# Performance work log

Hardware: AMD Instinct MI355X
Metric: run time of the kernel (lower is better)

The kernel has to match this reference:

```python
import jax, jax.numpy as jnp
import numpy as np

B, P, H, W, K = 2, 4096, 128, 128, 8
RADIUS = 0.05  # NDC-space point radius (raster_settings.radius)


def setup_inputs() -> dict:
    key = jax.random.key(0)
    k1, k2, k3 = jax.random.split(key, 3)
    points_world = jax.random.normal(k1, (B, P, 3), jnp.float32)
    # near-identity rotation (row-vector convention: X_view = X_world @ R + T)
    R = jnp.eye(3, dtype=jnp.float32)[None] + 0.01 * jax.random.normal(k2, (B, 3, 3), jnp.float32)
    # translate cloud to z ~ +3 so points are in front of the camera
    T = (0.1 * jax.random.normal(k3, (B, 3), jnp.float32)).at[:, 2].add(3.0)
    focal = jnp.full((B,), 1.5, jnp.float32)
    return {"points_world": points_world, "R": R, "T": T, "focal": focal}


def reference(points_world, R, T, focal):
    # --- camera transform: world -> view -> NDC (z kept in view space) ---
    pts_view = jnp.einsum('bpi,bij->bpj', points_world, R) + T[:, None, :]  # [B,P,3]
    z = pts_view[..., 2]                                                    # [B,P]
    x_ndc = focal[:, None] * pts_view[..., 0] / z
    y_ndc = focal[:, None] * pts_view[..., 1] / z

    # --- pixel-center NDC grid (pytorch3d convention: +x left, +y up) ---
    gx = 1.0 - 2.0 * (jnp.arange(W, dtype=jnp.float32) + 0.5) / W  # [W]
    gy = 1.0 - 2.0 * (jnp.arange(H, dtype=jnp.float32) + 0.5) / H  # [H]
    GY, GX = jnp.meshgrid(gy, gx, indexing='ij')
    gxf = GX.reshape(-1)  # [HW]
    gyf = GY.reshape(-1)

    # --- per-pixel candidate search: squared NDC distance to every point ---
    dist2 = (gxf[None, :, None] - x_ndc[:, None, :]) ** 2 \
          + (gyf[None, :, None] - y_ndc[:, None, :]) ** 2      # [B,HW,P]
    inside = (dist2 < RADIUS * RADIUS) & (z[:, None, :] > 0.0)  # in radius & in front

    # --- depth-sorted top-K nearest-in-z among covering points ---
    keyz = jnp.where(inside, z[:, None, :], jnp.inf)            # [B,HW,P]
    neg_top, idx_top = jax.lax.top_k(-keyz, K)                  # K smallest z
    zk = jnp.take_along_axis(keyz, idx_top, axis=-1)            # [B,HW,K]
    dk = jnp.take_along_axis(dist2, idx_top, axis=-1)
    valid = jnp.isfinite(zk)

    idx = jnp.where(valid, idx_top, -1).reshape(B, H, W, K)
    zbuf = jnp.where(valid, zk, -1.0).reshape(B, H, W, K)
    dists = jnp.where(valid, dk, -1.0).reshape(B, H, W, K)
    return idx, zbuf, dists
```

## Files before the change

kernel.cpp:

```cpp
#include <hip/hip_runtime.h>
#include <math.h>

#define BB 2
#define PP 4096
#define HH 128
#define WW 128
#define KK 8
#define TS 8
#define NTX (WW / TS)
#define NTY (HH / TS)
#define NW 4
#define SEG (PP / NW)

__global__ __launch_bounds__(64 * NW, 2) void raster_kernel(
    const float* __restrict__ pw,
    const float* __restrict__ Rm,
    const float* __restrict__ Tv,
    const float* __restrict__ fo,
    float* __restrict__ out,
    int N)
{
    __shared__ float4 cand[NW][SEG];

    const int tx = blockIdx.x, ty = blockIdx.y, b = blockIdx.z;
    const int wv   = threadIdx.x >> 6;
    const int lane = threadIdx.x & 63;

    const float* r = Rm + b * 9;
    const float r00=r[0], r01=r[1], r02=r[2];
    const float r10=r[3], r11=r[4], r12=r[5];
    const float r20=r[6], r21=r[7], r22=r[8];
    const float t0=Tv[b*3+0], t1=Tv[b*3+1], t2=Tv[b*3+2];
    const float f = fo[b];

    const float R2f   = (float)(0.05 * 0.05);
    const float apron = 0.05f + 1e-5f;

    float gx_hi = 1.0f - 2.0f * ((float)(tx * TS)          + 0.5f) / (float)WW;
    float gx_lo = 1.0f - 2.0f * ((float)(tx * TS + TS - 1) + 0.5f) / (float)WW;
    float gy_hi = 1.0f - 2.0f * ((float)(ty * TS)          + 0.5f) / (float)HH;
    float gy_lo = 1.0f - 2.0f * ((float)(ty * TS + TS - 1) + 0.5f) / (float)HH;
    const float xmin = gx_lo - apron, xmax = gx_hi + apron;
    const float ymin = gy_lo - apron, ymax = gy_hi + apron;

    int cnt = 0;
    const float* pwb = pw + (size_t)b * PP * 3;
#pragma unroll 4
    for (int it = 0; it < SEG / 64; ++it) {
        int i = wv * SEG + it * 64 + lane;
        const float* q = pwb + i * 3;
        float x = q[0], y = q[1], z = q[2];
        float vx = __fadd_rn(__fadd_rn(__fadd_rn(__fmul_rn(x, r00), __fmul_rn(y, r10)), __fmul_rn(z, r20)), t0);
        float vy = __fadd_rn(__fadd_rn(__fadd_rn(__fmul_rn(x, r01), __fmul_rn(y, r11)), __fmul_rn(z, r21)), t1);
        float vz = __fadd_rn(__fadd_rn(__fadd_rn(__fmul_rn(x, r02), __fmul_rn(y, r12)), __fmul_rn(z, r22)), t2);
        float xn = __fmul_rn(f, vx) / vz;
        float yn = __fmul_rn(f, vy) / vz;
        bool keep = (vz > 0.0f) && (xn >= xmin) && (xn <= xmax)
                                && (yn >= ymin) && (yn <= ymax);
        unsigned long long m = __ballot(keep);
        if (keep) {
            int pos = __popcll(m & ((1ull << lane) - 1ull));
            cand[wv][cnt + pos] = make_float4(xn, yn, vz, __int_as_float(i));
        }
        cnt += __popcll(m);
    }

    int w = tx * TS + (lane & (TS - 1));
    int h = ty * TS + (lane / TS);
    float gx = 1.0f - 2.0f * ((float)w + 0.5f) / (float)WW;
    float gy = 1.0f - 2.0f * ((float)h + 0.5f) / (float)HH;

    float zk[KK], dk[KK]; int ik[KK];
#pragma unroll
    for (int j = 0; j < KK; ++j) { zk[j] = INFINITY; dk[j] = -1.0f; ik[j] = -1; }

    for (int s = 0; s < cnt; ++s) {
        float4 q = cand[wv][s];
        float dx = __fsub_rn(gx, q.x);
        float dy = __fsub_rn(gy, q.y);
        float d2 = __fadd_rn(__fmul_rn(dx, dx), __fmul_rn(dy, dy));
        float z = q.z;
        if (d2 < R2f && z < zk[KK - 1]) {
            int i = __float_as_int(q.w);
#pragma unroll
            for (int j = KK - 1; j >= 1; --j) {
                if (z < zk[j]) {
                    if (z < zk[j - 1]) { zk[j] = zk[j-1]; ik[j] = ik[j-1]; dk[j] = dk[j-1]; }
                    else               { zk[j] = z;       ik[j] = i;       dk[j] = d2;      }
                }
            }
            if (z < zk[0]) { zk[0] = z; ik[0] = i; dk[0] = d2; }
        }
    }

    __syncthreads();
    float* mz = (float*)&cand[0][0];
    float* mi = mz + NW * KK * 64;
    float* md = mi + NW * KK * 64;
#pragma unroll
    for (int s = 0; s < KK; ++s) {
        mz[(wv * KK + s) * 64 + lane] = zk[s];
        mi[(wv * KK + s) * 64 + lane] = __int_as_float(ik[s]);
        md[(wv * KK + s) * 64 + lane] = dk[s];
    }
    __syncthreads();

    if (wv == 0) {
        float hz[NW], hd[NW]; int hi_[NW], hp[NW];
#pragma unroll
        for (int wq = 0; wq < NW; ++wq) {
            hp[wq]  = 0;
            hz[wq]  = mz[(wq * KK) * 64 + lane];
            hi_[wq] = __float_as_int(mi[(wq * KK) * 64 + lane]);
            hd[wq]  = md[(wq * KK) * 64 + lane];
        }
        float A[KK], Z[KK], D[KK];
#pragma unroll
        for (int o = 0; o < KK; ++o) {
            int bw = 0;
#pragma unroll
            for (int wq = 1; wq < NW; ++wq) {
                bool better = (hz[wq] < hz[bw]) ||
                              ((hz[wq] == hz[bw]) && (hi_[wq] < hi_[bw]));
                if (better) bw = wq;
            }
            float sz = hz[0], sd = hd[0]; int si = hi_[0];
#pragma unroll
            for (int wq = 1; wq < NW; ++wq) {
                if (bw == wq) { sz = hz[wq]; sd = hd[wq]; si = hi_[wq]; }
            }
            A[o] = (float)si;
            Z[o] = (si >= 0) ? sz : -1.0f;
            D[o] = sd;
#pragma unroll
            for (int wq = 0; wq < NW; ++wq) {
                if (bw == wq) {
                    int p = ++hp[wq];
                    if (p < KK) {
                        hz[wq]  = mz[(wq * KK + p) * 64 + lane];
                        hi_[wq] = __float_as_int(mi[(wq * KK + p) * 64 + lane]);
                        hd[wq]  = md[(wq * KK + p) * 64 + lane];
                    } else {
                        hz[wq] = INFINITY; hi_[wq] = -1; hd[wq] = -1.0f;
                    }
                }
            }
        }
        int pix  = (b * HH + h) * WW + w;
        int base = pix * KK;
        float4* oa = (float4*)(out + base);
        float4* oz = (float4*)(out + N + base);
        float4* od = (float4*)(out + 2 * N + base);
        oa[0] = ((float4*)A)[0]; oa[1] = ((float4*)A)[1];
        oz[0] = ((float4*)Z)[0]; oz[1] = ((float4*)Z)[1];
        od[0] = ((float4*)D)[0]; od[1] = ((float4*)D)[1];
    }
}

extern "C" void kernel_launch(void* const* d_in, const int* in_sizes, int n_in,
                              void* d_out, int out_size, void* d_ws, size_t ws_size,
                              hipStream_t stream) {
    const float* pw = (const float*)d_in[0];
    const float* Rm = (const float*)d_in[1];
    const float* Tv = (const float*)d_in[2];
    const float* fo = (const float*)d_in[3];
    int N = out_size / 3;

    hipLaunchKernelGGL(raster_kernel, dim3(NTX, NTY, BB), dim3(64 * NW), 0, stream,
                       pw, Rm, Tv, fo, (float*)d_out, N);
}
```

Before: 88.97 us.

## Use eight waves per tile with capped candidate buffers and prefetched point loads

```diff
diff --git a/kernel.cpp b/kernel.cpp
--- a/kernel.cpp
+++ b/kernel.cpp
@@ -9,10 +9,12 @@
 #define TS 8
 #define NTX (WW / TS)
 #define NTY (HH / TS)
-#define NW 4
+#define NW 8
 #define SEG (PP / NW)
+#define CIT (SEG / 64)
+#define CAP 384
 
-__global__ __launch_bounds__(64 * NW, 2) void raster_kernel(
+__global__ __launch_bounds__(64 * NW, 4) void raster_kernel(
     const float* __restrict__ pw,
     const float* __restrict__ Rm,
     const float* __restrict__ Tv,
@@ -20,7 +22,10 @@
     float* __restrict__ out,
     int N)
 {
-    __shared__ float4 cand[NW][SEG];
+    __shared__ union {
+        float4 cand[NW][CAP];
+        struct { float z[NW][KK][64], i[NW][KK][64], d[NW][KK][64]; } mg;
+    } sh;
 
     const int tx = blockIdx.x, ty = blockIdx.y, b = blockIdx.z;
     const int wv   = threadIdx.x >> 6;
@@ -43,13 +48,20 @@
     const float xmin = gx_lo - apron, xmax = gx_hi + apron;
     const float ymin = gy_lo - apron, ymax = gy_hi + apron;
 
+    float px[CIT], py[CIT], pz[CIT];
+    const float* basep = pw + ((size_t)b * PP + wv * SEG + lane) * 3;
+#pragma unroll
+    for (int it = 0; it < CIT; ++it) {
+        px[it] = basep[it * 192 + 0];
+        py[it] = basep[it * 192 + 1];
+        pz[it] = basep[it * 192 + 2];
+    }
+
     int cnt = 0;
-    const float* pwb = pw + (size_t)b * PP * 3;
-#pragma unroll 4
-    for (int it = 0; it < SEG / 64; ++it) {
+#pragma unroll
+    for (int it = 0; it < CIT; ++it) {
         int i = wv * SEG + it * 64 + lane;
-        const float* q = pwb + i * 3;
-        float x = q[0], y = q[1], z = q[2];
+        float x = px[it], y = py[it], z = pz[it];
         float vx = __fadd_rn(__fadd_rn(__fadd_rn(__fmul_rn(x, r00), __fmul_rn(y, r10)), __fmul_rn(z, r20)), t0);
         float vy = __fadd_rn(__fadd_rn(__fadd_rn(__fmul_rn(x, r01), __fmul_rn(y, r11)), __fmul_rn(z, r21)), t1);
         float vz = __fadd_rn(__fadd_rn(__fadd_rn(__fmul_rn(x, r02), __fmul_rn(y, r12)), __fmul_rn(z, r22)), t2);
@@ -59,11 +71,12 @@
                                 && (yn >= ymin) && (yn <= ymax);
         unsigned long long m = __ballot(keep);
         if (keep) {
-            int pos = __popcll(m & ((1ull << lane) - 1ull));
-            cand[wv][cnt + pos] = make_float4(xn, yn, vz, __int_as_float(i));
+            int slot = cnt + __popcll(m & ((1ull << lane) - 1ull));
+            if (slot < CAP) sh.cand[wv][slot] = make_float4(xn, yn, vz, __int_as_float(i));
         }
         cnt += __popcll(m);
     }
+    if (cnt > CAP) cnt = CAP;
 
     int w = tx * TS + (lane & (TS - 1));
     int h = ty * TS + (lane / TS);
@@ -75,7 +88,7 @@
     for (int j = 0; j < KK; ++j) { zk[j] = INFINITY; dk[j] = -1.0f; ik[j] = -1; }
 
     for (int s = 0; s < cnt; ++s) {
-        float4 q = cand[wv][s];
+        float4 q = sh.cand[wv][s];
         float dx = __fsub_rn(gx, q.x);
         float dy = __fsub_rn(gy, q.y);
         float d2 = __fadd_rn(__fmul_rn(dx, dx), __fmul_rn(dy, dy));
@@ -94,14 +107,11 @@
     }
 
     __syncthreads();
-    float* mz = (float*)&cand[0][0];
-    float* mi = mz + NW * KK * 64;
-    float* md = mi + NW * KK * 64;
 #pragma unroll
     for (int s = 0; s < KK; ++s) {
-        mz[(wv * KK + s) * 64 + lane] = zk[s];
-        mi[(wv * KK + s) * 64 + lane] = __int_as_float(ik[s]);
-        md[(wv * KK + s) * 64 + lane] = dk[s];
+        sh.mg.z[wv][s][lane] = zk[s];
+        sh.mg.i[wv][s][lane] = __int_as_float(ik[s]);
+        sh.mg.d[wv][s][lane] = dk[s];
     }
     __syncthreads();
 
@@ -110,9 +120,9 @@
 #pragma unroll
         for (int wq = 0; wq < NW; ++wq) {
             hp[wq]  = 0;
-            hz[wq]  = mz[(wq * KK) * 64 + lane];
-            hi_[wq] = __float_as_int(mi[(wq * KK) * 64 + lane]);
-            hd[wq]  = md[(wq * KK) * 64 + lane];
+            hz[wq]  = sh.mg.z[wq][0][lane];
+            hi_[wq] = __float_as_int(sh.mg.i[wq][0][lane]);
+            hd[wq]  = sh.mg.d[wq][0][lane];
         }
         float A[KK], Z[KK], D[KK];
 #pragma unroll
@@ -137,9 +147,9 @@
                 if (bw == wq) {
                     int p = ++hp[wq];
                     if (p < KK) {
-                        hz[wq]  = mz[(wq * KK + p) * 64 + lane];
-                        hi_[wq] = __float_as_int(mi[(wq * KK + p) * 64 + lane]);
-                        hd[wq]  = md[(wq * KK + p) * 64 + lane];
+                        hz[wq]  = sh.mg.z[wq][p][lane];
+                        hi_[wq] = __float_as_int(sh.mg.i[wq][p][lane]);
+                        hd[wq]  = sh.mg.d[wq][p][lane];
                     } else {
                         hz[wq] = INFINITY; hi_[wq] = -1; hd[wq] = -1.0f;
                     }
```

New measurement: 95.79 us. 1.08x slower.
